# Kernel optimization log

Measured on AMD Instinct MI355X. Metric: run time of the kernel, lower is better.

Reference implementation:

```python
import jax, jax.numpy as jnp
import numpy as np

SCALE = 8  # must match init_kwargs
B, H, W, C = 16, 256, 256, 64


def _nn_src_idx(dst_size, src_size):
    # TF2 tf.image.resize NEAREST uses half-pixel centers:
    # src = floor((dst + 0.5) * src_size / dst_size), clipped to valid range.
    idx = jnp.floor((jnp.arange(dst_size) + 0.5) * (src_size / dst_size)).astype(jnp.int32)
    return jnp.clip(idx, 0, src_size - 1)


def setup_inputs() -> dict:
    key = jax.random.key(0)
    x = jax.random.normal(key, (B, H, W, C), dtype=jnp.float32)
    return {"x": x}


def reference(x):
    b, h, w, c = x.shape
    s = SCALE
    # bin assignment of each pixel row/col (equivalent to NN-resizing the
    # scale x scale one-hot mask up to h x w)
    br = _nn_src_idx(h, s)  # [h] -> bin row in [0, s)
    bc = _nn_src_idx(w, s)  # [w] -> bin col in [0, s)
    R = jax.nn.one_hot(br, s, dtype=x.dtype)   # [h, s]
    Cm = jax.nn.one_hot(bc, s, dtype=x.dtype)  # [w, s]
    # spp[b,u,v,c] = (s^2 / (h*w)) * sum over pixels in bin (u,v) of x
    # (original: mean over all h*w pixels of masked tensor, times s^2)
    spp = jnp.einsum('bhwc,hu,wv->buvc', x, R, Cm) * (s * s / (h * w))
    # nearest-neighbor upsample back to (h, w)
    return spp[:, br][:, :, bc]
```

## Files before the change

### kernel.cpp

```cpp
#include <hip/hip_runtime.h>


__global__ __launch_bounds__(256) void spp_fused(const float4* __restrict__ x4,
                                                 float4* __restrict__ out4) {
    const int bin = blockIdx.x;
    const int v = bin & 7;
    const int u = (bin >> 3) & 7;
    const int b = bin >> 6;
    const int t = threadIdx.x;
    const int c4 = t & 15;
    const int rw = t >> 4;

    const int base = ((b * 256 + u * 32) * 256 + v * 32) * 16 + c4;
    const float4* __restrict__ src = x4 + base;

    float4 acc = make_float4(0.f, 0.f, 0.f, 0.f);
    #pragma unroll 8
    for (int k = 0; k < 64; ++k) {
        const int p = rw + (k << 4);
        const int r = p >> 5;
        const int q = p & 31;
        const float4 val = src[(r * 256 + q) * 16];
        acc.x += val.x; acc.y += val.y; acc.z += val.z; acc.w += val.w;
    }

    __shared__ float4 red[256];
    red[t] = acc;
    __syncthreads();
    for (int s = 8; s >= 1; s >>= 1) {
        if (rw < s) {
            const float4 o = red[(rw + s) * 16 + c4];
            float4 m = red[t];
            m.x += o.x; m.y += o.y; m.z += o.z; m.w += o.w;
            red[t] = m;
        }
        __syncthreads();
    }

    float4 m = red[c4];
    const float inv = 1.0f / 1024.0f;
    m.x *= inv; m.y *= inv; m.z *= inv; m.w *= inv;

    float4* __restrict__ dst = out4 + base;
    #pragma unroll 8
    for (int k = 0; k < 64; ++k) {
        const int p = rw + (k << 4);
        const int r = p >> 5;
        const int q = p & 31;
        dst[(r * 256 + q) * 16] = m;
    }
}

extern "C" void kernel_launch(void* const* d_in, const int* in_sizes, int n_in,
                              void* d_out, int out_size, void* d_ws, size_t ws_size,
                              hipStream_t stream) {
    const float4* x4   = (const float4*)d_in[0];
    float4*       out4 = (float4*)d_out;
    spp_fused<<<dim3(16 * 8 * 8), dim3(256), 0, stream>>>(x4, out4);
}
```

Measured before the change: 437.4 us.

## Use 512-thread blocks with nontemporal loads/stores and wave-shuffle reduction

Doubles the block to 512 threads so each thread handles one column of the 32x32 bin and strides over rows, cutting per-thread iterations from 64 to 32. Loads and stores now use nontemporal builtins to avoid polluting cache on streaming data. The cross-thread reduction moves from a full shared-memory tree to wave shuffles plus a small shared-memory tree across waves. The aim is more memory-level parallelism and less synchronisation overhead, though the larger block may lower occupancy.

```diff
diff --git a/kernel.cpp b/kernel.cpp
--- a/kernel.cpp
+++ b/kernel.cpp
@@ -1,60 +1,64 @@
 #include <hip/hip_runtime.h>
 
 
-__global__ __launch_bounds__(256) void spp_fused(const float4* __restrict__ x4,
-                                                 float4* __restrict__ out4) {
+typedef float f32x4 __attribute__((ext_vector_type(4)));
+
+__global__ __launch_bounds__(512) void spp_fused(const f32x4* __restrict__ x4,
+                                                 f32x4* __restrict__ out4) {
     const int bin = blockIdx.x;
     const int v = bin & 7;
     const int u = (bin >> 3) & 7;
     const int b = bin >> 6;
     const int t = threadIdx.x;
     const int c4 = t & 15;
-    const int rw = t >> 4;
+    const int ph = t >> 4;
 
-    const int base = ((b * 256 + u * 32) * 256 + v * 32) * 16 + c4;
-    const float4* __restrict__ src = x4 + base;
+    const int base = ((b * 256 + u * 32) * 256 + v * 32 + ph) * 16 + c4;
+    const f32x4* __restrict__ src = x4 + base;
 
-    float4 acc = make_float4(0.f, 0.f, 0.f, 0.f);
+    f32x4 acc = (f32x4)(0.f);
     #pragma unroll 8
-    for (int k = 0; k < 64; ++k) {
-        const int p = rw + (k << 4);
-        const int r = p >> 5;
-        const int q = p & 31;
-        const float4 val = src[(r * 256 + q) * 16];
-        acc.x += val.x; acc.y += val.y; acc.z += val.z; acc.w += val.w;
+    for (int k = 0; k < 32; ++k) {
+        acc += __builtin_nontemporal_load(src + k * 256 * 16);
     }
 
-    __shared__ float4 red[256];
-    red[t] = acc;
-    __syncthreads();
-    for (int s = 8; s >= 1; s >>= 1) {
-        if (rw < s) {
-            const float4 o = red[(rw + s) * 16 + c4];
-            float4 m = red[t];
-            m.x += o.x; m.y += o.y; m.z += o.z; m.w += o.w;
-            red[t] = m;
-        }
-        __syncthreads();
+    #pragma unroll
+    for (int m = 16; m <= 32; m <<= 1) {
+        acc.x += __shfl_xor(acc.x, m);
+        acc.y += __shfl_xor(acc.y, m);
+        acc.z += __shfl_xor(acc.z, m);
+        acc.w += __shfl_xor(acc.w, m);
     }
 
-    float4 m = red[c4];
-    const float inv = 1.0f / 1024.0f;
-    m.x *= inv; m.y *= inv; m.z *= inv; m.w *= inv;
+    __shared__ f32x4 red[8][16];
+    const int wave = t >> 6;
+    if ((t & 63) < 16) red[wave][c4] = acc;
+    __syncthreads();
+    if (t < 128) {
+        const int w = t >> 4;
+        for (int s = 4; s >= 1; s >>= 1) {
+            if (w < s) {
+                red[w][c4] += red[w + s][c4];
+            }
+            __syncthreads();
+        }
+    } else {
+        for (int s = 4; s >= 1; s >>= 1) __syncthreads();
+    }
 
-    float4* __restrict__ dst = out4 + base;
+    f32x4 m = red[0][c4] * (1.0f / 1024.0f);
+
+    f32x4* __restrict__ dst = out4 + base;
     #pragma unroll 8
-    for (int k = 0; k < 64; ++k) {
-        const int p = rw + (k << 4);
-        const int r = p >> 5;
-        const int q = p & 31;
-        dst[(r * 256 + q) * 16] = m;
+    for (int k = 0; k < 32; ++k) {
+        __builtin_nontemporal_store(m, dst + k * 256 * 16);
     }
 }
 
 extern "C" void kernel_launch(void* const* d_in, const int* in_sizes, int n_in,
                               void* d_out, int out_size, void* d_ws, size_t ws_size,
                               hipStream_t stream) {
-    const float4* x4   = (const float4*)d_in[0];
-    float4*       out4 = (float4*)d_out;
-    spp_fused<<<dim3(16 * 8 * 8), dim3(256), 0, stream>>>(x4, out4);
+    const f32x4* x4   = (const f32x4*)d_in[0];
+    f32x4*       out4 = (f32x4*)d_out;
+    spp_fused<<<dim3(16 * 8 * 8), dim3(512), 0, stream>>>(x4, out4);
 }
```

Result: no change. 442.7 us (+1.2%).
